# Kernel optimization log

Hardware: AMD Instinct MI355X
Metric: run time of the kernel (lower is better)

The kernel has to match this reference:

```python
import jax, jax.numpy as jnp
import numpy as np

EPS = 1e-5

def _layernorm(x, g, b):
    mu = jnp.mean(x, axis=-1, keepdims=True)
    var = jnp.mean(jnp.square(x - mu), axis=-1, keepdims=True)
    return (x - mu) * jax.lax.rsqrt(var + EPS) * g + b

def setup_inputs() -> dict:
    key = jax.random.key(0)
    ks = jax.random.split(key, 8)
    B, N, D, DFF = 64, 197, 768, 3072
    s = 0.02
    return {
        "x": jax.random.normal(ks[0], (B, N, D), jnp.float32),
        "ln1_g": jnp.ones((D,), jnp.float32),
        "ln1_b": jnp.zeros((D,), jnp.float32),
        "wq": jax.random.normal(ks[1], (D, D), jnp.float32) * s,
        "bq": jnp.zeros((D,), jnp.float32),
        "wk": jax.random.normal(ks[2], (D, D), jnp.float32) * s,
        "bk": jnp.zeros((D,), jnp.float32),
        "wv": jax.random.normal(ks[3], (D, D), jnp.float32) * s,
        "bv": jnp.zeros((D,), jnp.float32),
        "wo": jax.random.normal(ks[4], (D, D), jnp.float32) * s,
        "bo": jnp.zeros((D,), jnp.float32),
        "ln2_g": jnp.ones((D,), jnp.float32),
        "ln2_b": jnp.zeros((D,), jnp.float32),
        "w1": jax.random.normal(ks[5], (D, DFF), jnp.float32) * s,
        "b1": jnp.zeros((DFF,), jnp.float32),
        "w2": jax.random.normal(ks[6], (DFF, D), jnp.float32) * s,
        "b2": jnp.zeros((D,), jnp.float32),
    }

def reference(x, ln1_g, ln1_b, wq, bq, wk, bk, wv, bv, wo, bo,
              ln2_g, ln2_b, w1, b1, w2, b2):
    B, N, D = x.shape
    H = 12
    hd = D // H
    scale = hd ** -0.5
    # layer_norm1 + qkv projection (disable_reuse path: no reuse module)
    h = _layernorm(x, ln1_g, ln1_b)
    q = (h @ wq + bq).reshape(B, N, H, hd) * scale
    k = (h @ wk + bk).reshape(B, N, H, hd)
    v = (h @ wv + bv).reshape(B, N, H, hd)
    # manual bmm attention, full [B,H,N,N] probs materialized & returned
    qk = jnp.einsum('bqhd,bkhd->bhqk', q, k)
    attn_weights = jax.nn.softmax(qk, axis=-1)
    attn = jnp.einsum('bhqk,bkhd->bqhd', attn_weights, v)
    pre_proj = attn.reshape(B, N, D)
    hs = x + (pre_proj @ wo + bo)
    # MLP block
    residual = hs
    h2 = _layernorm(hs, ln2_g, ln2_b)
    h2 = jax.nn.gelu(h2 @ w1 + b1, approximate=False)
    hidden_states = residual + (h2 @ w2 + b2)
    # reuse_start == 'before_mlp': (pre_proj, cache_states=None, hidden, attn_w, qkvs=None, reuse_map=None)
    return (pre_proj, hidden_states, attn_weights)
```

## Files before the change

kernel.cpp:

```cpp
#include <hip/hip_runtime.h>
#include <math.h>

typedef unsigned short u16;
typedef __bf16 bf16x8 __attribute__((ext_vector_type(8)));
typedef float f32x4 __attribute__((ext_vector_type(4)));

#define MROWS 12608
#define NSEQ  197
#define NHEAD 12
#define DMODEL 768

__device__ __forceinline__ u16 f2bf(float f) {
    __bf16 h = (__bf16)f;
    return __builtin_bit_cast(u16, h);
}
__device__ __forceinline__ float bf2f(u16 v) { return __uint_as_float(((unsigned)v) << 16); }

__device__ __forceinline__ bf16x8 cvt8(const float* p) {
    float4 a = *(const float4*)p;
    float4 b = *(const float4*)(p + 4);
    union { bf16x8 v; u16 s[8]; } t;
    t.s[0] = f2bf(a.x); t.s[1] = f2bf(a.y); t.s[2] = f2bf(a.z); t.s[3] = f2bf(a.w);
    t.s[4] = f2bf(b.x); t.s[5] = f2bf(b.y); t.s[6] = f2bf(b.z); t.s[7] = f2bf(b.w);
    return t.v;
}

__device__ __forceinline__ void g2l16(const u16* g, u16* l) {
    __builtin_amdgcn_global_load_lds((const __attribute__((address_space(1))) unsigned*)g,
                                     (__attribute__((address_space(3))) unsigned*)l,
                                     16, 0, 0);
}

__device__ __forceinline__ bool xcd_decode(int& x, int& y) {
    int bid = blockIdx.x;
    int c = bid & 7, j = bid >> 3;
    int cnt = (c < 3) ? 13 : 12;
    int x0  = (c < 3) ? c * 13 : 39 + (c - 3) * 12;
    y = j / 13;
    int xi = j - y * 13;
    if (xi >= cnt) return false;
    x = x0 + xi;
    return true;
}

__global__ __launch_bounds__(256) void ln_rows(const float* x,
                                               const float* g,
                                               const float* bta,
                                               u16* o, int Mr) {
    int w = threadIdx.x >> 6, lane = threadIdx.x & 63;
    int row = blockIdx.x * 4 + w;
    if (row >= Mr) return;
    const float* xr = x + (size_t)row * DMODEL;
    float vals[12];
    for (int i = 0; i < 6; ++i) {
        float2 xx = *(const float2*)(xr + i * 128 + lane * 2);
        vals[2 * i] = xx.x; vals[2 * i + 1] = xx.y;
    }
    float s = 0.f;
    for (int i = 0; i < 12; ++i) s += vals[i];
    for (int off = 1; off < 64; off <<= 1) s += __shfl_xor(s, off, 64);
    float mu = s * (1.f / 768.f);
    float v2 = 0.f;
    for (int i = 0; i < 12; ++i) { float d = vals[i] - mu; v2 += d * d; }
    for (int off = 1; off < 64; off <<= 1) v2 += __shfl_xor(v2, off, 64);
    float rstd = rsqrtf(v2 * (1.f / 768.f) + 1e-5f);
    u16* orow = o + (size_t)row * DMODEL;
    for (int i = 0; i < 6; ++i) {
        int c = i * 128 + lane * 2;
        float2 gg = *(const float2*)(g + c);
        float2 bb = *(const float2*)(bta + c);
        float y0 = (vals[2 * i] - mu) * rstd * gg.x + bb.x;
        float y1 = (vals[2 * i + 1] - mu) * rstd * gg.y + bb.y;
        *(unsigned*)(orow + c) = (unsigned)f2bf(y0) | ((unsigned)f2bf(y1) << 16);
    }
}

__global__ __launch_bounds__(256) void wtrans(const float* __restrict__ src,
                                              u16* __restrict__ dst,
                                              int ldsrc, int lddst) {
    __shared__ float t[32][33];
    int c = threadIdx.x & 31, r0 = threadIdx.x >> 5;
    int k0 = blockIdx.x * 32, n0 = blockIdx.y * 32;
#pragma unroll
    for (int i = 0; i < 4; ++i)
        t[r0 + 8 * i][c] = src[(size_t)(k0 + r0 + 8 * i) * ldsrc + n0 + c];
    __syncthreads();
#pragma unroll
    for (int i = 0; i < 4; ++i)
        dst[(size_t)(n0 + r0 + 8 * i) * lddst + k0 + c] = f2bf(t[c][r0 + 8 * i]);
}

__device__ __forceinline__ void gemm_core128(
    const u16* __restrict__ A, const u16* __restrict__ BT,
    int M, int K, int lda, int ldb, int x, int y,
    u16* aT, u16* bT, f32x4 (&acc)[4][4])
{
    int tid = threadIdx.x, w = tid >> 6, lane = tid & 63;
    int row0 = x * 128, col0 = y * 128;
    int rsub = lane >> 2;
    int kch = ((lane & 3) ^ ((rsub >> 1) & 3)) * 8;

    const u16* aG[2]; const u16* bG[2]; int lof[2];
#pragma unroll
    for (int i = 0; i < 2; ++i) {
        int g = (w * 2 + i) * 16 + rsub;
        int gr = row0 + g; if (gr > M - 1) gr = M - 1;
        aG[i] = A + (size_t)gr * lda + kch;
        bG[i] = BT + (size_t)(col0 + g) * ldb + kch;
        lof[i] = (w * 2 + i) * 512;
    }

    const f32x4 z = {0.f, 0.f, 0.f, 0.f};
#pragma unroll
    for (int i = 0; i < 4; ++i)
#pragma unroll
        for (int j = 0; j < 4; ++j) acc[i][j] = z;

#pragma unroll
    for (int i = 0; i < 2; ++i) { g2l16(aG[i], aT + lof[i]); g2l16(bG[i], bT + lof[i]); }
    __syncthreads();

    int lrow = lane & 15, lq = lane >> 4;
    int rof = (lq ^ ((lrow >> 1) & 3)) * 8;
    int wm = w >> 1, wn = w & 1;
    int nt = K >> 5;
    for (int t = 0; t < nt; ++t) {
        int cur = (t & 1) * 4096;
        if (t + 1 < nt) {
            int nx = 4096 - cur, ko = (t + 1) << 5;
#pragma unroll
            for (int i = 0; i < 2; ++i) {
                g2l16(aG[i] + ko, aT + nx + lof[i]);
                g2l16(bG[i] + ko, bT + nx + lof[i]);
            }
        }
        const u16* aC = aT + cur;
        const u16* bC = bT + cur;
        bf16x8 af[4], bfr[4];
#pragma unroll
        for (int mt = 0; mt < 4; ++mt)
            af[mt] = *(const bf16x8*)(aC + (wm * 64 + mt * 16 + lrow) * 32 + rof);
#pragma unroll
        for (int n2 = 0; n2 < 4; ++n2)
            bfr[n2] = *(const bf16x8*)(bC + (wn * 64 + n2 * 16 + lrow) * 32 + rof);
#pragma unroll
        for (int mt = 0; mt < 4; ++mt)
#pragma unroll
            for (int n2 = 0; n2 < 4; ++n2)
                acc[mt][n2] = __builtin_amdgcn_mfma_f32_16x16x32_bf16(af[mt], bfr[n2], acc[mt][n2], 0, 0, 0);
        __syncthreads();
    }
}

__global__ __launch_bounds__(256) void gemm_std(
    const u16* __restrict__ A, const u16* __restrict__ BT,
    float* Cf, u16* Cb, const float* bias, const float* resid,
    int M, int K, int lda, int ldb, int ldc, float scale, int do_gelu)
{
    __shared__ __align__(16) u16 aT[2 * 4096];
    __shared__ __align__(16) u16 bT[2 * 4096];
    int x, y;
    if (!xcd_decode(x, y)) return;
    f32x4 acc[4][4];
    gemm_core128(A, BT, M, K, lda, ldb, x, y, aT, bT, acc);

    int tid = threadIdx.x, w = tid >> 6, lane = tid & 63;
    int row0 = x * 128, col0 = y * 128;
    int wmB = (w >> 1) * 64, wnB = (w & 1) * 64;
    int lrow = lane & 15, lq = lane >> 4;
#pragma unroll
    for (int mt = 0; mt < 4; ++mt) {
        int gmb = row0 + wmB + mt * 16 + lq * 4;
#pragma unroll
        for (int n2 = 0; n2 < 4; ++n2) {
            int gc = col0 + wnB + n2 * 16 + lrow;
            float bv = bias ? bias[gc] : 0.f;
            for (int r = 0; r < 4; ++r) {
                int gm = gmb + r;
                if (gm < M) {
                    float v0 = (acc[mt][n2][r] + bv) * scale;
                    if (do_gelu) v0 = 0.5f * v0 * (1.f + erff(v0 * 0.70710678118654752f));
                    if (resid) v0 += resid[(size_t)gm * ldc + gc];
                    if (Cf) Cf[(size_t)gm * ldc + gc] = v0;
                    if (Cb) Cb[(size_t)gm * ldc + gc] = f2bf(v0);
                }
            }
        }
    }
}

__global__ __launch_bounds__(256) void gemm_qkv(
    const u16* __restrict__ A, const u16* __restrict__ BT,
    float* qo, float* ko, u16* vo,
    const float* bq, const float* bk, const float* bvv, int M)
{
    __shared__ __align__(16) u16 aT[2 * 4096];
    __shared__ __align__(16) u16 bT[2 * 4096];
    int x, y;
    if (!xcd_decode(x, y)) return;
    f32x4 acc[4][4];
    gemm_core128(A, BT, M, 768, 768, 768, x, y, aT, bT, acc);

    int tid = threadIdx.x, w = tid >> 6, lane = tid & 63;
    int row0 = x * 128, col0 = y * 128;
    int wmB = (w >> 1) * 64, wnB = (w & 1) * 64;
    int lrow = lane & 15, lq = lane >> 4;
#pragma unroll
    for (int mt = 0; mt < 4; ++mt) {
        int gmb = row0 + wmB + mt * 16 + lq * 4;
#pragma unroll
        for (int n2 = 0; n2 < 4; ++n2) {
            int gc = col0 + wnB + n2 * 16 + lrow;
            int j = gc / 768;
            int c = gc - j * 768;
            const float* bp = (j == 0) ? bq : (j == 1) ? bk : bvv;
            float bb = bp[c];
            for (int r = 0; r < 4; ++r) {
                int gm = gmb + r;
                if (gm < M) {
                    float v0 = acc[mt][n2][r] + bb;
                    size_t off = (size_t)gm * 768 + c;
                    if (j == 0)      qo[off] = v0 * 0.125f;
                    else if (j == 1) ko[off] = v0;
                    else             vo[off] = f2bf(v0);
                }
            }
        }
    }
}

__global__ __launch_bounds__(256) void attn_fused(const float* q, const float* k,
                                                  const u16* v, float* attnw,
                                                  float* outf, u16* outb) {
    __shared__ __align__(16) u16 vT[64 * 224];
    __shared__ __align__(16) u16 P[4][16 * 224];
    int bid = blockIdx.x;
    int bh = bid >> 1, mb = bid & 1;
    int b = bh / NHEAD, hh = bh - b * NHEAD;
    int tid = threadIdx.x, w = tid >> 6, lane = tid & 63;
    int lrow = lane & 15, lq = lane >> 4;

    {
        int cg = (tid & 7) * 8;
        int rb = tid >> 3;
        for (int i = 0; i < 7; ++i) {
            int r = rb + i * 32;
            union { uint4 qv; u16 s[8]; } tmp;
            if (r < 197) {
                tmp.qv = *(const uint4*)(v + (size_t)(b * NSEQ + r) * DMODEL + hh * 64 + cg);
            } else {
                tmp.qv.x = tmp.qv.y = tmp.qv.z = tmp.qv.w = 0u;
            }
            for (int j = 0; j < 8; ++j) vT[(cg + j) * 224 + r] = tmp.s[j];
        }
    }
    u16* Pw = &P[w][0];
#pragma unroll
    for (int r = 0; r < 4; ++r) {
        int m = lq * 4 + r;
        Pw[m * 224 + ((208 + lrow) ^ (lq << 3))] = 0;
    }
    __syncthreads();

    size_t pbase = (size_t)bh * (NSEQ * NSEQ);
    int mstart = mb ? 7 : 0;
    int mcount = mb ? 6 : 7;

    for (int round = 0; round < 2; ++round) {
        int mi = round * 4 + w;
        if (mi >= mcount) continue;
        int mtile = mstart + mi;

        int gm0 = mtile * 16 + lrow; int gmq = gm0 > 196 ? 196 : gm0;
        const float* qrow = q + (size_t)(b * NSEQ + gmq) * DMODEL + hh * 64;
        bf16x8 aq0 = cvt8(qrow + lq * 8);
        bf16x8 aq1 = cvt8(qrow + 32 + lq * 8);

        f32x4 s[13];
#pragma unroll
        for (int nt = 0; nt < 13; ++nt) {
            int gn = nt * 16 + lrow; if (gn > 196) gn = 196;
            const float* krow = k + (size_t)(b * NSEQ + gn) * DMODEL + hh * 64;
            bf16x8 bk0 = cvt8(krow + lq * 8);
            bf16x8 bk1 = cvt8(krow + 32 + lq * 8);
            f32x4 a = {0.f, 0.f, 0.f, 0.f};
            a = __builtin_amdgcn_mfma_f32_16x16x32_bf16(aq0, bk0, a, 0, 0, 0);
            a = __builtin_amdgcn_mfma_f32_16x16x32_bf16(aq1, bk1, a, 0, 0, 0);
            s[nt] = a;
        }

        float rls[4];
        bool colbad = (lrow >= 5);
#pragma unroll
        for (int r = 0; r < 4; ++r) {
            float m1 = -1e30f;
#pragma unroll
            for (int nt = 0; nt < 12; ++nt) m1 = fmaxf(m1, s[nt][r]);
            m1 = fmaxf(m1, colbad ? -1e30f : s[12][r]);
            m1 = fmaxf(m1, __shfl_xor(m1, 1, 64));
            m1 = fmaxf(m1, __shfl_xor(m1, 2, 64));
            m1 = fmaxf(m1, __shfl_xor(m1, 4, 64));
            m1 = fmaxf(m1, __shfl_xor(m1, 8, 64));
            float sm = 0.f;
#pragma unroll
            for (int nt = 0; nt < 13; ++nt) {
                float e = __expf(s[nt][r] - m1);
                if (nt == 12 && colbad) e = 0.f;
                s[nt][r] = e;
                sm += e;
            }
            sm += __shfl_xor(sm, 1, 64);
            sm += __shfl_xor(sm, 2, 64);
            sm += __shfl_xor(sm, 4, 64);
            sm += __shfl_xor(sm, 8, 64);
            rls[r] = 1.f / sm;
        }

#pragma unroll
        for (int nt = 0; nt < 13; ++nt) {
            int gc = nt * 16 + lrow;
            bool cok = (gc < 197);
#pragma unroll
            for (int r = 0; r < 4; ++r) {
                float p = s[nt][r] * rls[r];
                s[nt][r] = p;
                int gm = mtile * 16 + lq * 4 + r;
                if (cok && gm < 197)
                    attnw[pbase + (size_t)gm * 197 + gc] = p;
            }
        }
#pragma unroll
        for (int nt = 0; nt < 13; ++nt) {
#pragma unroll
            for (int r = 0; r < 4; ++r) {
                int m = lq * 4 + r;
                Pw[m * 224 + ((nt * 16 + lrow) ^ (lq << 3))] = f2bf(s[nt][r]);
            }
        }

        f32x4 o[4];
        const f32x4 zf = {0.f, 0.f, 0.f, 0.f};
#pragma unroll
        for (int n2 = 0; n2 < 4; ++n2) o[n2] = zf;
#pragma unroll
        for (int ks = 0; ks < 7; ++ks) {
            bf16x8 af = *(const bf16x8*)(Pw + lrow * 224 + ((ks * 32 + lq * 8) ^ ((lrow >> 2) << 3)));
#pragma unroll
            for (int n2 = 0; n2 < 4; ++n2) {
                bf16x8 bv = *(const bf16x8*)(&vT[(n2 * 16 + lrow) * 224 + ks * 32 + lq * 8]);
                o[n2] = __builtin_amdgcn_mfma_f32_16x16x32_bf16(af, bv, o[n2], 0, 0, 0);
            }
        }
#pragma unroll
        for (int n2 = 0; n2 < 4; ++n2) {
            int gcol = hh * 64 + n2 * 16 + lrow;
#pragma unroll
            for (int r = 0; r < 4; ++r) {
                int gm = mtile * 16 + lq * 4 + r;
                if (gm < 197) {
                    size_t off = (size_t)(b * NSEQ + gm) * DMODEL + gcol;
                    outf[off] = o[n2][r];
                    outb[off] = f2bf(o[n2][r]);
                }
            }
        }
    }
}

extern "C" void kernel_launch(void* const* d_in, const int* in_sizes, int n_in,
                              void* d_out, int out_size, void* d_ws, size_t ws_size,
                              hipStream_t stream) {
    const float* x    = (const float*)d_in[0];
    const float* ln1g = (const float*)d_in[1];
    const float* ln1b = (const float*)d_in[2];
    const float* wq   = (const float*)d_in[3];
    const float* bq   = (const float*)d_in[4];
    const float* wk   = (const float*)d_in[5];
    const float* bk   = (const float*)d_in[6];
    const float* wv   = (const float*)d_in[7];
    const float* bv   = (const float*)d_in[8];
    const float* wo   = (const float*)d_in[9];
    const float* bo   = (const float*)d_in[10];
    const float* ln2g = (const float*)d_in[11];
    const float* ln2b = (const float*)d_in[12];
    const float* w1   = (const float*)d_in[13];
    const float* b1   = (const float*)d_in[14];
    const float* w2   = (const float*)d_in[15];
    const float* b2   = (const float*)d_in[16];

    float* out     = (float*)d_out;
    float* preproj = out;
    float* hidden  = out + 9682944;
    float* attnw   = out + 19365888;

    u16* bufA = (u16*)d_ws;
    u16* bufB = bufA + 9682944;

    u16* qkvT = (u16*)attnw;

    long long tailElems = (long long)(ws_size >> 1) - 19365888LL;
    int CH; u16* w1T;
    if (tailElems >= 1179648LL)      { CH = 768; w1T = bufB + 9682944; }
    else if (tailElems >= 786432LL)  { CH = 512; w1T = bufB + 9682944; }
    else                             { CH = 512; w1T = bufB + 6455296; }
    u16* w2T = w1T + (size_t)CH * 768;
    int NCH = 3072 / CH;

    ln_rows<<<3152, 256, 0, stream>>>(x, ln1g, ln1b, bufA, MROWS);
    wtrans<<<dim3(24, 24), 256, 0, stream>>>(wq, qkvT,           768, 768);
    wtrans<<<dim3(24, 24), 256, 0, stream>>>(wk, qkvT + 589824,  768, 768);
    wtrans<<<dim3(24, 24), 256, 0, stream>>>(wv, qkvT + 1179648, 768, 768);
    gemm_qkv<<<104 * 18, 256, 0, stream>>>(bufA, qkvT, preproj, hidden, bufB,
                                           bq, bk, bv, MROWS);
    attn_fused<<<1536, 256, 0, stream>>>(preproj, hidden, bufB, attnw, preproj, bufA);
    wtrans<<<dim3(24, 24), 256, 0, stream>>>(wo, bufB, 768, 768);
    gemm_std<<<104 * 6, 256, 0, stream>>>(bufA, bufB, hidden, nullptr, bo, x,
                                          MROWS, 768, 768, 768, 768, 1.f, 0);
    ln_rows<<<3152, 256, 0, stream>>>(hidden, ln2g, ln2b, bufA, MROWS);
    for (int ci = 0; ci < NCH; ++ci) {
        wtrans<<<dim3(24, CH / 32), 256, 0, stream>>>(w1 + ci * CH, w1T, 3072, 768);
        wtrans<<<dim3(CH / 32, 24), 256, 0, stream>>>(w2 + (size_t)ci * CH * 768, w2T, 768, CH);
        gemm_std<<<104 * (CH / 128), 256, 0, stream>>>(
            bufA, w1T, nullptr, bufB, b1 + ci * CH, nullptr,
            MROWS, 768, 768, 768, CH, 1.f, 1);
        gemm_std<<<104 * 6, 256, 0, stream>>>(
            bufB, w2T, hidden, nullptr, (ci == 0) ? b2 : nullptr, hidden,
            MROWS, CH, CH, CH, 768, 1.f, 0);
    }
}
```

Baseline: 922.1 us.

## Batch all weight transposes into one launch and unchunk the MLP GEMMs

Adds a single wtrans_all kernel that transposes and converts all six weight matrices in one launch. When the workspace is large enough, the MLP runs as one full-width GELU GEMM followed by one full-K down-projection, instead of a loop over hidden-dimension chunks. This removes many small launches and the repeated read-modify-write of the hidden output across chunks. In exchange it needs a much larger workspace to hold the full intermediate activation and all transposed weights, and it falls back to the old chunked path otherwise.

```diff
diff --git a/kernel.cpp b/kernel.cpp
--- a/kernel.cpp
+++ b/kernel.cpp
@@ -81,6 +81,42 @@
     __shared__ float t[32][33];
     int c = threadIdx.x & 31, r0 = threadIdx.x >> 5;
     int k0 = blockIdx.x * 32, n0 = blockIdx.y * 32;
+#pragma unroll
+    for (int i = 0; i < 4; ++i)
+        t[r0 + 8 * i][c] = src[(size_t)(k0 + r0 + 8 * i) * ldsrc + n0 + c];
+    __syncthreads();
+#pragma unroll
+    for (int i = 0; i < 4; ++i)
+        dst[(size_t)(n0 + r0 + 8 * i) * lddst + k0 + c] = f2bf(t[c][r0 + 8 * i]);
+}
+
+__global__ __launch_bounds__(256) void wtrans_all(
+    const float* __restrict__ wq, const float* __restrict__ wk,
+    const float* __restrict__ wv, const float* __restrict__ wo,
+    const float* __restrict__ w1, const float* __restrict__ w2,
+    u16* qkvT, u16* woT, u16* w1T, u16* w2T)
+{
+    int bid = blockIdx.x;
+    const float* src; u16* dst; int ldsrc, lddst, k0, n0;
+    if (bid < 2304) {
+        int which = bid / 576, e = bid - which * 576;
+        k0 = (e % 24) * 32; n0 = (e / 24) * 32;
+        ldsrc = 768; lddst = 768;
+        if (which == 0)      { src = wq; dst = qkvT; }
+        else if (which == 1) { src = wk; dst = qkvT + 589824; }
+        else if (which == 2) { src = wv; dst = qkvT + 1179648; }
+        else                 { src = wo; dst = woT; }
+    } else if (bid < 4608) {
+        int e = bid - 2304;
+        k0 = (e % 24) * 32; n0 = (e / 24) * 32;
+        src = w1; dst = w1T; ldsrc = 3072; lddst = 768;
+    } else {
+        int e = bid - 4608;
+        k0 = (e % 96) * 32; n0 = (e / 96) * 32;
+        src = w2; dst = w2T; ldsrc = 768; lddst = 3072;
+    }
+    __shared__ float t[32][33];
+    int c = threadIdx.x & 31, r0 = threadIdx.x >> 5;
 #pragma unroll
     for (int i = 0; i < 4; ++i)
         t[r0 + 8 * i][c] = src[(size_t)(k0 + r0 + 8 * i) * ldsrc + n0 + c];
@@ -395,36 +431,58 @@
 
     u16* bufA = (u16*)d_ws;
     u16* bufB = bufA + 9682944;
-
     u16* qkvT = (u16*)attnw;
 
     long long tailElems = (long long)(ws_size >> 1) - 19365888LL;
-    int CH; u16* w1T;
-    if (tailElems >= 1179648LL)      { CH = 768; w1T = bufB + 9682944; }
-    else if (tailElems >= 786432LL)  { CH = 512; w1T = bufB + 9682944; }
-    else                             { CH = 512; w1T = bufB + 6455296; }
-    u16* w2T = w1T + (size_t)CH * 768;
-    int NCH = 3072 / CH;
+    u16* tail = bufB + 9682944;
 
     ln_rows<<<3152, 256, 0, stream>>>(x, ln1g, ln1b, bufA, MROWS);
-    wtrans<<<dim3(24, 24), 256, 0, stream>>>(wq, qkvT,           768, 768);
-    wtrans<<<dim3(24, 24), 256, 0, stream>>>(wk, qkvT + 589824,  768, 768);
-    wtrans<<<dim3(24, 24), 256, 0, stream>>>(wv, qkvT + 1179648, 768, 768);
-    gemm_qkv<<<104 * 18, 256, 0, stream>>>(bufA, qkvT, preproj, hidden, bufB,
-                                           bq, bk, bv, MROWS);
-    attn_fused<<<1536, 256, 0, stream>>>(preproj, hidden, bufB, attnw, preproj, bufA);
-    wtrans<<<dim3(24, 24), 256, 0, stream>>>(wo, bufB, 768, 768);
-    gemm_std<<<104 * 6, 256, 0, stream>>>(bufA, bufB, hidden, nullptr, bo, x,
-                                          MROWS, 768, 768, 768, 768, 1.f, 0);
-    ln_rows<<<3152, 256, 0, stream>>>(hidden, ln2g, ln2b, bufA, MROWS);
-    for (int ci = 0; ci < NCH; ++ci) {
-        wtrans<<<dim3(24, CH / 32), 256, 0, stream>>>(w1 + ci * CH, w1T, 3072, 768);
-        wtrans<<<dim3(CH / 32, 24), 256, 0, stream>>>(w2 + (size_t)ci * CH * 768, w2T, 768, CH);
-        gemm_std<<<104 * (CH / 128), 256, 0, stream>>>(
-            bufA, w1T, nullptr, bufB, b1 + ci * CH, nullptr,
-            MROWS, 768, 768, 768, CH, 1.f, 1);
-        gemm_std<<<104 * 6, 256, 0, stream>>>(
-            bufB, w2T, hidden, nullptr, (ci == 0) ? b2 : nullptr, hidden,
-            MROWS, CH, CH, CH, 768, 1.f, 0);
-    }
-}
+
+    if (tailElems >= 44015616LL) {
+        u16* woT  = tail;
+        u16* w1T  = woT + 589824;
+        u16* w2T  = w1T + 2359296;
+        u16* gelu = w2T + 2359296;
+
+        wtrans_all<<<6912, 256, 0, stream>>>(wq, wk, wv, wo, w1, w2,
+                                             qkvT, woT, w1T, w2T);
+        gemm_qkv<<<104 * 18, 256, 0, stream>>>(bufA, qkvT, preproj, hidden, bufB,
+                                               bq, bk, bv, MROWS);
+        attn_fused<<<1536, 256, 0, stream>>>(preproj, hidden, bufB, attnw, preproj, bufA);
+        gemm_std<<<104 * 6, 256, 0, stream>>>(bufA, woT, hidden, nullptr, bo, x,
+                                              MROWS, 768, 768, 768, 768, 1.f, 0);
+        ln_rows<<<3152, 256, 0, stream>>>(hidden, ln2g, ln2b, bufA, MROWS);
+        gemm_std<<<104 * 24, 256, 0, stream>>>(bufA, w1T, nullptr, gelu, b1, nullptr,
+                                               MROWS, 768, 768, 768, 3072, 1.f, 1);
+        gemm_std<<<104 * 6, 256, 0, stream>>>(gelu, w2T, hidden, nullptr, b2, hidden,
+                                              MROWS, 3072, 3072, 3072, 768, 1.f, 0);
+    } else {
+        int CH; u16* w1T;
+        if (tailElems >= 1179648LL)      { CH = 768; w1T = tail; }
+        else if (tailElems >= 786432LL)  { CH = 512; w1T = tail; }
+        else                             { CH = 512; w1T = bufB + 6455296; }
+        u16* w2T = w1T + (size_t)CH * 768;
+        int NCH = 3072 / CH;
+
+        wtrans<<<dim3(24, 24), 256, 0, stream>>>(wq, qkvT,           768, 768);
+        wtrans<<<dim3(24, 24), 256, 0, stream>>>(wk, qkvT + 589824,  768, 768);
+        wtrans<<<dim3(24, 24), 256, 0, stream>>>(wv, qkvT + 1179648, 768, 768);
+        gemm_qkv<<<104 * 18, 256, 0, stream>>>(bufA, qkvT, preproj, hidden, bufB,
+                                               bq, bk, bv, MROWS);
+        attn_fused<<<1536, 256, 0, stream>>>(preproj, hidden, bufB, attnw, preproj, bufA);
+        wtrans<<<dim3(24, 24), 256, 0, stream>>>(wo, bufB, 768, 768);
+        gemm_std<<<104 * 6, 256, 0, stream>>>(bufA, bufB, hidden, nullptr, bo, x,
+                                              MROWS, 768, 768, 768, 768, 1.f, 0);
+        ln_rows<<<3152, 256, 0, stream>>>(hidden, ln2g, ln2b, bufA, MROWS);
+        for (int ci = 0; ci < NCH; ++ci) {
+            wtrans<<<dim3(24, CH / 32), 256, 0, stream>>>(w1 + ci * CH, w1T, 3072, 768);
+            wtrans<<<dim3(CH / 32, 24), 256, 0, stream>>>(w2 + (size_t)ci * CH * 768, w2T, 768, CH);
+            gemm_std<<<104 * (CH / 128), 256, 0, stream>>>(
+                bufA, w1T, nullptr, bufB, b1 + ci * CH, nullptr,
+                MROWS, 768, 768, 768, CH, 1.f, 1);
+            gemm_std<<<104 * 6, 256, 0, stream>>>(
+                bufB, w2T, hidden, nullptr, (ci == 0) ? b2 : nullptr, hidden,
+                MROWS, CH, CH, CH, 768, 1.f, 0);
+        }
+    }
+}
```

New measurement: 803.2 us. 1.15x faster.
